# Optimization experiments

Hardware: AMD Instinct MI355X
Metric: run time of the kernel (lower is better)

## Reference

```python
import jax, jax.numpy as jnp
import numpy as np
import math

B, L, H, E = 4, 1024, 8, 64

def setup_inputs() -> dict:
    key = jax.random.key(0)
    kq, kk, kv, ks = jax.random.split(key, 4)
    return {
        "queries": jax.random.normal(kq, (B, L, H, E), dtype=jnp.float32),
        "keys": jax.random.normal(kk, (B, L, H, E), dtype=jnp.float32),
        "values": jax.random.normal(kv, (B, L, H, E), dtype=jnp.float32),
        "sigma": jax.random.normal(ks, (B, L, H), dtype=jnp.float32),
    }

def reference(queries, keys, values, sigma):
    b, l, h, e = queries.shape
    scale = 1.0 / math.sqrt(e)
    # QK^T scores: [B,H,L,S]
    scores = jnp.einsum('blhe,bshe->bhls', queries, keys)
    # triangular causal mask (mask_flag=True, attn_mask=None path)
    causal = jnp.triu(jnp.ones((l, l), dtype=bool), k=1)
    scores = jnp.where(causal[None, None], -jnp.inf, scores)
    attn = scale * scores
    # sigma -> Gaussian prior
    sig = jnp.transpose(sigma, (0, 2, 1))                      # [B,H,L]
    sig = jax.nn.sigmoid(sig * 5.0) + 1e-5
    sig = jnp.power(3.0, sig) - 1.0
    sig = jnp.broadcast_to(sig[..., None], (b, h, l, l))       # [B,H,L,L]
    idx = jnp.arange(l)
    dist = jnp.abs(idx[:, None] - idx[None, :]).astype(jnp.float32)  # [L,L]
    inv_sqrt_2pi = 1.0 / math.sqrt(2.0 * math.pi)
    prior = inv_sqrt_2pi / sig * jnp.exp(-(dist ** 2) / 2.0 / (sig ** 2))
    series = jax.nn.softmax(attn, axis=-1)                     # dropout p=0 -> identity
    V = jnp.einsum('bhls,bshd->blhd', series, values)
    return V, series, prior, sig
```

## Files before the change

### kernel.cpp

```cpp
#include <hip/hip_runtime.h>

typedef __attribute__((ext_vector_type(8))) short bf16x8;
typedef __attribute__((ext_vector_type(4))) float f32x4;

constexpr int NB = 4, NL = 1024, NH = 8, NE = 64, NBH = NB * NH;

constexpr size_t OFF_V      = 0;
constexpr size_t OFF_SERIES = (size_t)NB * NL * NH * NE;
constexpr size_t OFF_PRIOR  = OFF_SERIES + (size_t)NBH * NL * NL;
constexpr size_t OFF_SIG    = OFF_PRIOR  + (size_t)NBH * NL * NL;

__device__ __forceinline__ unsigned short f2bf(float x) {
  unsigned int u = __builtin_bit_cast(unsigned int, x);
  u = (u + 0x7FFFu + ((u >> 16) & 1u)) >> 16;
  return (unsigned short)u;
}

__device__ __forceinline__ f32x4 mfma16(bf16x8 a, bf16x8 b, f32x4 c) {
  return __builtin_amdgcn_mfma_f32_16x16x32_bf16(a, b, c, 0, 0, 0);
}

__global__ __launch_bounds__(256)
void prior_kernel(const float* __restrict__ sigma, float* __restrict__ out) {
  const float inv_sqrt_2pi = 0.39894228040143267f;
  const float ln3 = 1.0986122886681098f;
  float4* __restrict__ prior4  = (float4*)(out + OFF_PRIOR);
  float4* __restrict__ sig4    = (float4*)(out + OFF_SIG);
  float4* __restrict__ series4 = (float4*)(out + OFF_SERIES);

  const int tid  = threadIdx.x;
  const int lane = tid & 63;
  const int rowIdx = blockIdx.x * 4 + (tid >> 6);
  const int l  = rowIdx & 1023;
  const int bh = rowIdx >> 10;
  const int b  = bh >> 3, h = bh & 7;

  const float x    = sigma[((size_t)b * NL + l) * NH + h];
  const float sg   = 1.0f / (1.0f + __expf(-5.0f * x)) + 1e-5f;
  const float sigv = __expf(sg * ln3) - 1.0f;
  const float coef = inv_sqrt_2pi / sigv;
  const float inv2 = -0.5f / (sigv * sigv);

  const size_t rbase = (size_t)rowIdx * (NL / 4);
  const int rbe4 = ((l & ~63) + 64) >> 2;
  const float4 zero4 = make_float4(0.f, 0.f, 0.f, 0.f);
  const float4 sv = make_float4(sigv, sigv, sigv, sigv);

#pragma unroll
  for (int k = 0; k < 4; ++k) {
    const int c  = lane + k * 64;
    const int sb = c * 4;
    const int d0 = l - sb, d1 = l - (sb + 1), d2 = l - (sb + 2), d3 = l - (sb + 3);
    float4 pr;
    pr.x = coef * __expf((float)(d0 * d0) * inv2);
    pr.y = coef * __expf((float)(d1 * d1) * inv2);
    pr.z = coef * __expf((float)(d2 * d2) * inv2);
    pr.w = coef * __expf((float)(d3 * d3) * inv2);
    prior4[rbase + c] = pr;
    sig4[rbase + c]   = sv;
    if (c >= rbe4) series4[rbase + c] = zero4;
  }
}

__device__ __forceinline__ void stage64(const float* __restrict__ src,
                                        unsigned short* lds) {
  const int t = threadIdx.x;
  const int s = t >> 2, q = t & 3;
  const float4* rp = (const float4*)(src + (size_t)s * (NH * NE) + q * 16);
  float4 v0 = rp[0], v1 = rp[1], v2 = rp[2], v3 = rp[3];
  unsigned int u[8];
  u[0] = f2bf(v0.x) | ((unsigned)f2bf(v0.y) << 16);
  u[1] = f2bf(v0.z) | ((unsigned)f2bf(v0.w) << 16);
  u[2] = f2bf(v1.x) | ((unsigned)f2bf(v1.y) << 16);
  u[3] = f2bf(v1.z) | ((unsigned)f2bf(v1.w) << 16);
  u[4] = f2bf(v2.x) | ((unsigned)f2bf(v2.y) << 16);
  u[5] = f2bf(v2.z) | ((unsigned)f2bf(v2.w) << 16);
  u[6] = f2bf(v3.x) | ((unsigned)f2bf(v3.y) << 16);
  u[7] = f2bf(v3.z) | ((unsigned)f2bf(v3.w) << 16);
  const int sw = (s & 7) << 4;
  char* row = (char*)lds + s * 128;
  *(uint4*)(row + ((q * 32)      ^ sw)) = make_uint4(u[0], u[1], u[2], u[3]);
  *(uint4*)(row + ((q * 32 + 16) ^ sw)) = make_uint4(u[4], u[5], u[6], u[7]);
}

__device__ __forceinline__ void stageV(const float* __restrict__ src,
                                       unsigned int* ldsv) {
  const int t = threadIdx.x;
  const int sp = t >> 3;
  const int ec = t & 7;
  const float* r0 = src + (size_t)(2 * sp) * (NH * NE) + ec * 8;
  const float* r1 = r0 + NH * NE;
  float4 a0 = ((const float4*)r0)[0], a1 = ((const float4*)r0)[1];
  float4 b0 = ((const float4*)r1)[0], b1 = ((const float4*)r1)[1];
  unsigned int u[8];
  u[0] = f2bf(a0.x) | ((unsigned)f2bf(b0.x) << 16);
  u[1] = f2bf(a0.y) | ((unsigned)f2bf(b0.y) << 16);
  u[2] = f2bf(a0.z) | ((unsigned)f2bf(b0.z) << 16);
  u[3] = f2bf(a0.w) | ((unsigned)f2bf(b0.w) << 16);
  u[4] = f2bf(a1.x) | ((unsigned)f2bf(b1.x) << 16);
  u[5] = f2bf(a1.y) | ((unsigned)f2bf(b1.y) << 16);
  u[6] = f2bf(a1.z) | ((unsigned)f2bf(b1.z) << 16);
  u[7] = f2bf(a1.w) | ((unsigned)f2bf(b1.w) << 16);
  unsigned int* p = ldsv + sp * 68 + ec * 8;
  *(uint4*)(p)     = make_uint4(u[0], u[1], u[2], u[3]);
  *(uint4*)(p + 4) = make_uint4(u[4], u[5], u[6], u[7]);
}

__device__ __forceinline__ bf16x8 readAB(const unsigned short* lds, int row,
                                         int bytecol) {
  const char* p = (const char*)lds + row * 128 + (bytecol ^ ((row & 7) << 4));
  return *(const bf16x8*)p;
}

__global__ __launch_bounds__(256)
void attn_kernel(const float* __restrict__ Qp, const float* __restrict__ Kp,
                 const float* __restrict__ Vp, float* __restrict__ out) {
  const int blk = blockIdx.x;
  const int bh = blk & 31;
  const int g5 = blk >> 5;
  const int w  = (g5 < 8) ? (15 - g5) : (g5 - 8);
  const int b = bh >> 3, h = bh & 7;

  __shared__ unsigned short ldsQ[64 * 64];
  __shared__ unsigned short ldsK[64 * 64];
  __shared__ unsigned int   ldsV[32 * 68];
  __shared__ unsigned short ldsP[4][16 * 72];
  const int tid  = threadIdx.x;
  const int lane = tid & 63;
  const int wv   = tid >> 6;
  const int g    = lane >> 4;
  const int e0   = lane & 15;

  const size_t rowstride = NH * NE;
  const float* Qbase = Qp + ((size_t)(b * NL + w * 64) * NH + h) * NE;
  const float* Kbase = Kp + ((size_t)(b * NL) * NH + h) * NE;
  const float* Vbase = Vp + ((size_t)(b * NL) * NH + h) * NE;

  stage64(Qbase, ldsQ);
  __syncthreads();

  const bf16x8 aq0 = readAB(ldsQ, wv * 16 + e0, g * 16);
  const bf16x8 aq1 = readAB(ldsQ, wv * 16 + e0, g * 16 + 64);

  const float scale = 0.125f;
  const int r_glob0 = w * 64 + wv * 16 + g * 4;
  float rsum[4] = {0.f, 0.f, 0.f, 0.f};

  for (int st = 0; st <= w; ++st) {
    __syncthreads();
    stage64(Kbase + (size_t)(st * 64) * rowstride, ldsK);
    __syncthreads();
#pragma unroll
    for (int ct = 0; ct < 4; ++ct) {
      f32x4 acc = {0.f, 0.f, 0.f, 0.f};
      bf16x8 bk0 = readAB(ldsK, ct * 16 + e0, g * 16);
      bf16x8 bk1 = readAB(ldsK, ct * 16 + e0, g * 16 + 64);
      acc = mfma16(aq0, bk0, acc);
      acc = mfma16(aq1, bk1, acc);
      const int s_g = st * 64 + ct * 16 + e0;
#pragma unroll
      for (int j = 0; j < 4; ++j) {
        float e = __expf(acc[j] * scale - 20.0f);
        if (s_g > r_glob0 + j) e = 0.f;
        rsum[j] += e;
      }
    }
  }

  float rinv[4];
#pragma unroll
  for (int j = 0; j < 4; ++j) {
    float v = rsum[j];
    v += __shfl_xor(v, 1);
    v += __shfl_xor(v, 2);
    v += __shfl_xor(v, 4);
    v += __shfl_xor(v, 8);
    rinv[j] = 1.0f / v;
  }

  f32x4 acc_o[4];
#pragma unroll
  for (int i = 0; i < 4; ++i) acc_o[i] = f32x4{0.f, 0.f, 0.f, 0.f};

  unsigned short* ldsPw = ldsP[wv];
  float* __restrict__ series = out + OFF_SERIES + (size_t)bh * NL * NL;

  for (int st = 0; st <= w; ++st) {
    __syncthreads();
    stage64(Kbase + (size_t)(st * 64) * rowstride, ldsK);
    stageV (Vbase + (size_t)(st * 64) * rowstride, ldsV);
    __syncthreads();
#pragma unroll
    for (int ct = 0; ct < 4; ++ct) {
      f32x4 acc = {0.f, 0.f, 0.f, 0.f};
      bf16x8 bk0 = readAB(ldsK, ct * 16 + e0, g * 16);
      bf16x8 bk1 = readAB(ldsK, ct * 16 + e0, g * 16 + 64);
      acc = mfma16(aq0, bk0, acc);
      acc = mfma16(aq1, bk1, acc);
      const int s_g = st * 64 + ct * 16 + e0;
#pragma unroll
      for (int j = 0; j < 4; ++j) {
        float e = __expf(acc[j] * scale - 20.0f);
        if (s_g > r_glob0 + j) e = 0.f;
        const float pn = e * rinv[j];
        series[(size_t)(r_glob0 + j) * NL + s_g] = pn;
        ldsPw[(g * 4 + j) * 72 + ct * 16 + e0] = f2bf(pn);
      }
    }
#pragma unroll
    for (int sh = 0; sh < 2; ++sh) {
      const char* pp = (const char*)ldsPw + e0 * 144 + sh * 64 + g * 16;
      const bf16x8 ap = *(const bf16x8*)pp;
#pragma unroll
      for (int ce = 0; ce < 4; ++ce) {
        const unsigned int* vp = ldsV + (sh * 16 + g * 4) * 68 + ce * 16 + e0;
        uint4 vw = make_uint4(vp[0], vp[68], vp[136], vp[204]);
        const bf16x8 bv = __builtin_bit_cast(bf16x8, vw);
        acc_o[ce] = mfma16(ap, bv, acc_o[ce]);
      }
    }
  }

  float* __restrict__ vout = out + OFF_V;
#pragma unroll
  for (int ce = 0; ce < 4; ++ce) {
#pragma unroll
    for (int j = 0; j < 4; ++j) {
      vout[((size_t)(b * NL + r_glob0 + j) * NH + h) * NE + ce * 16 + e0] =
          acc_o[ce][j];
    }
  }
}

extern "C" void kernel_launch(void* const* d_in, const int* in_sizes, int n_in,
                              void* d_out, int out_size, void* d_ws, size_t ws_size,
                              hipStream_t stream) {
  const float* Qp = (const float*)d_in[0];
  const float* Kp = (const float*)d_in[1];
  const float* Vp = (const float*)d_in[2];
  const float* Sg = (const float*)d_in[3];
  float* out = (float*)d_out;
  (void)d_ws; (void)ws_size;

  prior_kernel<<<dim3(NBH * NL / 4), dim3(256), 0, stream>>>(Sg, out);
  attn_kernel <<<dim3(512),          dim3(256), 0, stream>>>(Qp, Kp, Vp, out);
}
```

Baseline: 460.8 us.

## Single-pass attention writing unnormalized series, normalize in prior kernel

Removes the first QK^T pass that only computed row sums. The attention kernel now writes unnormalized exp scores to series and accumulates PV unnormalized, scaling V by the reciprocal sum at the end. It stores per-row reciprocals in the workspace, which the prior kernel (now launched second) uses to rescale series with a read-modify-write. The change also adds register prefetch of the next K/V tile and s_setprio around the PV MFMAs. The cost is an extra read and write of the lower-triangular series in the prior kernel, in exchange for halving the QK^T and exp work.

```diff
diff --git a/kernel.cpp b/kernel.cpp
--- a/kernel.cpp
+++ b/kernel.cpp
@@ -20,8 +20,188 @@
   return __builtin_amdgcn_mfma_f32_16x16x32_bf16(a, b, c, 0, 0, 0);
 }
 
+__device__ __forceinline__ void loadT(const float* __restrict__ src, float4* r) {
+  const int t = threadIdx.x;
+  const int s = t >> 2, q = t & 3;
+  const float4* rp = (const float4*)(src + (size_t)s * (NH * NE) + q * 16);
+  r[0] = rp[0]; r[1] = rp[1]; r[2] = rp[2]; r[3] = rp[3];
+}
+
+__device__ __forceinline__ void writeT(const float4* v, unsigned short* lds) {
+  const int t = threadIdx.x;
+  const int s = t >> 2, q = t & 3;
+  unsigned int u[8];
+  u[0] = f2bf(v[0].x) | ((unsigned)f2bf(v[0].y) << 16);
+  u[1] = f2bf(v[0].z) | ((unsigned)f2bf(v[0].w) << 16);
+  u[2] = f2bf(v[1].x) | ((unsigned)f2bf(v[1].y) << 16);
+  u[3] = f2bf(v[1].z) | ((unsigned)f2bf(v[1].w) << 16);
+  u[4] = f2bf(v[2].x) | ((unsigned)f2bf(v[2].y) << 16);
+  u[5] = f2bf(v[2].z) | ((unsigned)f2bf(v[2].w) << 16);
+  u[6] = f2bf(v[3].x) | ((unsigned)f2bf(v[3].y) << 16);
+  u[7] = f2bf(v[3].z) | ((unsigned)f2bf(v[3].w) << 16);
+  const int sw = (s & 7) << 4;
+  char* row = (char*)lds + s * 128;
+  *(uint4*)(row + ((q * 32)      ^ sw)) = make_uint4(u[0], u[1], u[2], u[3]);
+  *(uint4*)(row + ((q * 32 + 16) ^ sw)) = make_uint4(u[4], u[5], u[6], u[7]);
+}
+
+__device__ __forceinline__ void loadV(const float* __restrict__ src, float4* r) {
+  const int t = threadIdx.x;
+  const int sp = t >> 3, ec = t & 7;
+  const float* r0 = src + (size_t)(2 * sp) * (NH * NE) + ec * 8;
+  const float* r1 = r0 + NH * NE;
+  r[0] = ((const float4*)r0)[0]; r[1] = ((const float4*)r0)[1];
+  r[2] = ((const float4*)r1)[0]; r[3] = ((const float4*)r1)[1];
+}
+
+__device__ __forceinline__ void writeV(const float4* v, unsigned int* ldsv) {
+  const int t = threadIdx.x;
+  const int sp = t >> 3, ec = t & 7;
+  unsigned int u[8];
+  u[0] = f2bf(v[0].x) | ((unsigned)f2bf(v[2].x) << 16);
+  u[1] = f2bf(v[0].y) | ((unsigned)f2bf(v[2].y) << 16);
+  u[2] = f2bf(v[0].z) | ((unsigned)f2bf(v[2].z) << 16);
+  u[3] = f2bf(v[0].w) | ((unsigned)f2bf(v[2].w) << 16);
+  u[4] = f2bf(v[1].x) | ((unsigned)f2bf(v[3].x) << 16);
+  u[5] = f2bf(v[1].y) | ((unsigned)f2bf(v[3].y) << 16);
+  u[6] = f2bf(v[1].z) | ((unsigned)f2bf(v[3].z) << 16);
+  u[7] = f2bf(v[1].w) | ((unsigned)f2bf(v[3].w) << 16);
+  unsigned int* p = ldsv + sp * 68 + ec * 8;
+  *(uint4*)(p)     = make_uint4(u[0], u[1], u[2], u[3]);
+  *(uint4*)(p + 4) = make_uint4(u[4], u[5], u[6], u[7]);
+}
+
+__device__ __forceinline__ void stageQ(const float* __restrict__ src,
+                                       unsigned short* lds) {
+  float4 r[4];
+  loadT(src, r);
+  writeT(r, lds);
+}
+
+__device__ __forceinline__ bf16x8 readAB(const unsigned short* lds, int row,
+                                         int bytecol) {
+  const char* p = (const char*)lds + row * 128 + (bytecol ^ ((row & 7) << 4));
+  return *(const bf16x8*)p;
+}
+
 __global__ __launch_bounds__(256)
-void prior_kernel(const float* __restrict__ sigma, float* __restrict__ out) {
+void attn_kernel(const float* __restrict__ Qp, const float* __restrict__ Kp,
+                 const float* __restrict__ Vp, float* __restrict__ rws,
+                 float* __restrict__ out) {
+  const int blk = blockIdx.x;
+  const int bh = blk & 31;
+  const int g5 = blk >> 5;
+  const int w  = (g5 < 8) ? (15 - g5) : (g5 - 8);
+  const int b = bh >> 3, h = bh & 7;
+
+  __shared__ unsigned short ldsQ[64 * 64];
+  __shared__ unsigned short ldsK[64 * 64];
+  __shared__ unsigned int   ldsV[32 * 68];
+  __shared__ unsigned short ldsP[4][16 * 72];
+
+  const int tid  = threadIdx.x;
+  const int lane = tid & 63;
+  const int wv   = tid >> 6;
+  const int g    = lane >> 4;
+  const int e0   = lane & 15;
+
+  const size_t rowstride = NH * NE;
+  const float* Qbase = Qp + ((size_t)(b * NL + w * 64) * NH + h) * NE;
+  const float* Kbase = Kp + ((size_t)(b * NL) * NH + h) * NE;
+  const float* Vbase = Vp + ((size_t)(b * NL) * NH + h) * NE;
+
+  stageQ(Qbase, ldsQ);
+  __syncthreads();
+
+  const bf16x8 aq0 = readAB(ldsQ, wv * 16 + e0, g * 16);
+  const bf16x8 aq1 = readAB(ldsQ, wv * 16 + e0, g * 16 + 64);
+
+  const float scale = 0.125f;
+  const int r_glob0 = w * 64 + wv * 16 + g * 4;
+  float rsum[4] = {0.f, 0.f, 0.f, 0.f};
+
+  f32x4 acc_o[4];
+#pragma unroll
+  for (int i = 0; i < 4; ++i) acc_o[i] = f32x4{0.f, 0.f, 0.f, 0.f};
+
+  unsigned short* ldsPw = ldsP[wv];
+  float* __restrict__ series = out + OFF_SERIES + (size_t)bh * NL * NL;
+
+  float4 kreg[4], vreg[4];
+  loadT(Kbase, kreg);
+  loadV(Vbase, vreg);
+
+  for (int st = 0; st <= w; ++st) {
+    __syncthreads();
+    writeT(kreg, ldsK);
+    writeV(vreg, ldsV);
+    __syncthreads();
+    if (st < w) {
+      loadT(Kbase + (size_t)((st + 1) * 64) * rowstride, kreg);
+      loadV(Vbase + (size_t)((st + 1) * 64) * rowstride, vreg);
+    }
+#pragma unroll
+    for (int ct = 0; ct < 4; ++ct) {
+      f32x4 acc = {0.f, 0.f, 0.f, 0.f};
+      bf16x8 bk0 = readAB(ldsK, ct * 16 + e0, g * 16);
+      bf16x8 bk1 = readAB(ldsK, ct * 16 + e0, g * 16 + 64);
+      acc = mfma16(aq0, bk0, acc);
+      acc = mfma16(aq1, bk1, acc);
+      const int s_g = st * 64 + ct * 16 + e0;
+#pragma unroll
+      for (int j = 0; j < 4; ++j) {
+        float e = __expf(acc[j] * scale - 20.0f);
+        if (s_g > r_glob0 + j) e = 0.f;
+        rsum[j] += e;
+        series[(size_t)(r_glob0 + j) * NL + s_g] = e;
+        ldsPw[(g * 4 + j) * 72 + ct * 16 + e0] = f2bf(e);
+      }
+    }
+    __builtin_amdgcn_s_setprio(1);
+#pragma unroll
+    for (int sh = 0; sh < 2; ++sh) {
+      const char* pp = (const char*)ldsPw + e0 * 144 + sh * 64 + g * 16;
+      const bf16x8 ap = *(const bf16x8*)pp;
+#pragma unroll
+      for (int ce = 0; ce < 4; ++ce) {
+        const unsigned int* vp = ldsV + (sh * 16 + g * 4) * 68 + ce * 16 + e0;
+        uint4 vw = make_uint4(vp[0], vp[68], vp[136], vp[204]);
+        const bf16x8 bv = __builtin_bit_cast(bf16x8, vw);
+        acc_o[ce] = mfma16(ap, bv, acc_o[ce]);
+      }
+    }
+    __builtin_amdgcn_s_setprio(0);
+  }
+
+  float rinv[4];
+#pragma unroll
+  for (int j = 0; j < 4; ++j) {
+    float v = rsum[j];
+    v += __shfl_xor(v, 1);
+    v += __shfl_xor(v, 2);
+    v += __shfl_xor(v, 4);
+    v += __shfl_xor(v, 8);
+    rinv[j] = 1.0f / v;
+  }
+  if (e0 == 0) {
+#pragma unroll
+    for (int j = 0; j < 4; ++j) rws[(size_t)bh * NL + r_glob0 + j] = rinv[j];
+  }
+
+  float* __restrict__ vout = out + OFF_V;
+#pragma unroll
+  for (int ce = 0; ce < 4; ++ce) {
+#pragma unroll
+    for (int j = 0; j < 4; ++j) {
+      vout[((size_t)(b * NL + r_glob0 + j) * NH + h) * NE + ce * 16 + e0] =
+          acc_o[ce][j] * rinv[j];
+    }
+  }
+}
+
+__global__ __launch_bounds__(256)
+void prior_norm_kernel(const float* __restrict__ sigma,
+                       const float* __restrict__ rws, float* __restrict__ out) {
   const float inv_sqrt_2pi = 0.39894228040143267f;
   const float ln3 = 1.0986122886681098f;
   float4* __restrict__ prior4  = (float4*)(out + OFF_PRIOR);
@@ -40,6 +220,7 @@
   const float sigv = __expf(sg * ln3) - 1.0f;
   const float coef = inv_sqrt_2pi / sigv;
   const float inv2 = -0.5f / (sigv * sigv);
+  const float rinv = rws[rowIdx];
 
   const size_t rbase = (size_t)rowIdx * (NL / 4);
   const int rbe4 = ((l & ~63) + 64) >> 2;
@@ -58,176 +239,12 @@
     pr.w = coef * __expf((float)(d3 * d3) * inv2);
     prior4[rbase + c] = pr;
     sig4[rbase + c]   = sv;
-    if (c >= rbe4) series4[rbase + c] = zero4;
-  }
-}
-
-__device__ __forceinline__ void stage64(const float* __restrict__ src,
-                                        unsigned short* lds) {
-  const int t = threadIdx.x;
-  const int s = t >> 2, q = t & 3;
-  const float4* rp = (const float4*)(src + (size_t)s * (NH * NE) + q * 16);
-  float4 v0 = rp[0], v1 = rp[1], v2 = rp[2], v3 = rp[3];
-  unsigned int u[8];
-  u[0] = f2bf(v0.x) | ((unsigned)f2bf(v0.y) << 16);
-  u[1] = f2bf(v0.z) | ((unsigned)f2bf(v0.w) << 16);
-  u[2] = f2bf(v1.x) | ((unsigned)f2bf(v1.y) << 16);
-  u[3] = f2bf(v1.z) | ((unsigned)f2bf(v1.w) << 16);
-  u[4] = f2bf(v2.x) | ((unsigned)f2bf(v2.y) << 16);
-  u[5] = f2bf(v2.z) | ((unsigned)f2bf(v2.w) << 16);
-  u[6] = f2bf(v3.x) | ((unsigned)f2bf(v3.y) << 16);
-  u[7] = f2bf(v3.z) | ((unsigned)f2bf(v3.w) << 16);
-  const int sw = (s & 7) << 4;
-  char* row = (char*)lds + s * 128;
-  *(uint4*)(row + ((q * 32)      ^ sw)) = make_uint4(u[0], u[1], u[2], u[3]);
-  *(uint4*)(row + ((q * 32 + 16) ^ sw)) = make_uint4(u[4], u[5], u[6], u[7]);
-}
-
-__device__ __forceinline__ void stageV(const float* __restrict__ src,
-                                       unsigned int* ldsv) {
-  const int t = threadIdx.x;
-  const int sp = t >> 3;
-  const int ec = t & 7;
-  const float* r0 = src + (size_t)(2 * sp) * (NH * NE) + ec * 8;
-  const float* r1 = r0 + NH * NE;
-  float4 a0 = ((const float4*)r0)[0], a1 = ((const float4*)r0)[1];
-  float4 b0 = ((const float4*)r1)[0], b1 = ((const float4*)r1)[1];
-  unsigned int u[8];
-  u[0] = f2bf(a0.x) | ((unsigned)f2bf(b0.x) << 16);
-  u[1] = f2bf(a0.y) | ((unsigned)f2bf(b0.y) << 16);
-  u[2] = f2bf(a0.z) | ((unsigned)f2bf(b0.z) << 16);
-  u[3] = f2bf(a0.w) | ((unsigned)f2bf(b0.w) << 16);
-  u[4] = f2bf(a1.x) | ((unsigned)f2bf(b1.x) << 16);
-  u[5] = f2bf(a1.y) | ((unsigned)f2bf(b1.y) << 16);
-  u[6] = f2bf(a1.z) | ((unsigned)f2bf(b1.z) << 16);
-  u[7] = f2bf(a1.w) | ((unsigned)f2bf(b1.w) << 16);
-  unsigned int* p = ldsv + sp * 68 + ec * 8;
-  *(uint4*)(p)     = make_uint4(u[0], u[1], u[2], u[3]);
-  *(uint4*)(p + 4) = make_uint4(u[4], u[5], u[6], u[7]);
-}
-
-__device__ __forceinline__ bf16x8 readAB(const unsigned short* lds, int row,
-                                         int bytecol) {
-  const char* p = (const char*)lds + row * 128 + (bytecol ^ ((row & 7) << 4));
-  return *(const bf16x8*)p;
-}
-
-__global__ __launch_bounds__(256)
-void attn_kernel(const float* __restrict__ Qp, const float* __restrict__ Kp,
-                 const float* __restrict__ Vp, float* __restrict__ out) {
-  const int blk = blockIdx.x;
-  const int bh = blk & 31;
-  const int g5 = blk >> 5;
-  const int w  = (g5 < 8) ? (15 - g5) : (g5 - 8);
-  const int b = bh >> 3, h = bh & 7;
-
-  __shared__ unsigned short ldsQ[64 * 64];
-  __shared__ unsigned short ldsK[64 * 64];
-  __shared__ unsigned int   ldsV[32 * 68];
-  __shared__ unsigned short ldsP[4][16 * 72];
-  const int tid  = threadIdx.x;
-  const int lane = tid & 63;
-  const int wv   = tid >> 6;
-  const int g    = lane >> 4;
-  const int e0   = lane & 15;
-
-  const size_t rowstride = NH * NE;
-  const float* Qbase = Qp + ((size_t)(b * NL + w * 64) * NH + h) * NE;
-  const float* Kbase = Kp + ((size_t)(b * NL) * NH + h) * NE;
-  const float* Vbase = Vp + ((size_t)(b * NL) * NH + h) * NE;
-
-  stage64(Qbase, ldsQ);
-  __syncthreads();
-
-  const bf16x8 aq0 = readAB(ldsQ, wv * 16 + e0, g * 16);
-  const bf16x8 aq1 = readAB(ldsQ, wv * 16 + e0, g * 16 + 64);
-
-  const float scale = 0.125f;
-  const int r_glob0 = w * 64 + wv * 16 + g * 4;
-  float rsum[4] = {0.f, 0.f, 0.f, 0.f};
-
-  for (int st = 0; st <= w; ++st) {
-    __syncthreads();
-    stage64(Kbase + (size_t)(st * 64) * rowstride, ldsK);
-    __syncthreads();
-#pragma unroll
-    for (int ct = 0; ct < 4; ++ct) {
-      f32x4 acc = {0.f, 0.f, 0.f, 0.f};
-      bf16x8 bk0 = readAB(ldsK, ct * 16 + e0, g * 16);
-      bf16x8 bk1 = readAB(ldsK, ct * 16 + e0, g * 16 + 64);
-      acc = mfma16(aq0, bk0, acc);
-      acc = mfma16(aq1, bk1, acc);
-      const int s_g = st * 64 + ct * 16 + e0;
-#pragma unroll
-      for (int j = 0; j < 4; ++j) {
-        float e = __expf(acc[j] * scale - 20.0f);
-        if (s_g > r_glob0 + j) e = 0.f;
-        rsum[j] += e;
-      }
-    }
-  }
-
-  float rinv[4];
-#pragma unroll
-  for (int j = 0; j < 4; ++j) {
-    float v = rsum[j];
-    v += __shfl_xor(v, 1);
-    v += __shfl_xor(v, 2);
-    v += __shfl_xor(v, 4);
-    v += __shfl_xor(v, 8);
-    rinv[j] = 1.0f / v;
-  }
-
-  f32x4 acc_o[4];
-#pragma unroll
-  for (int i = 0; i < 4; ++i) acc_o[i] = f32x4{0.f, 0.f, 0.f, 0.f};
-
-  unsigned short* ldsPw = ldsP[wv];
-  float* __restrict__ series = out + OFF_SERIES + (size_t)bh * NL * NL;
-
-  for (int st = 0; st <= w; ++st) {
-    __syncthreads();
-    stage64(Kbase + (size_t)(st * 64) * rowstride, ldsK);
-    stageV (Vbase + (size_t)(st * 64) * rowstride, ldsV);
-    __syncthreads();
-#pragma unroll
-    for (int ct = 0; ct < 4; ++ct) {
-      f32x4 acc = {0.f, 0.f, 0.f, 0.f};
-      bf16x8 bk0 = readAB(ldsK, ct * 16 + e0, g * 16);
-      bf16x8 bk1 = readAB(ldsK, ct * 16 + e0, g * 16 + 64);
-      acc = mfma16(aq0, bk0, acc);
-      acc = mfma16(aq1, bk1, acc);
-      const int s_g = st * 64 + ct * 16 + e0;
-#pragma unroll
-      for (int j = 0; j < 4; ++j) {
-        float e = __expf(acc[j] * scale - 20.0f);
-        if (s_g > r_glob0 + j) e = 0.f;
-        const float pn = e * rinv[j];
-        series[(size_t)(r_glob0 + j) * NL + s_g] = pn;
-        ldsPw[(g * 4 + j) * 72 + ct * 16 + e0] = f2bf(pn);
-      }
-    }
-#pragma unroll
-    for (int sh = 0; sh < 2; ++sh) {
-      const char* pp = (const char*)ldsPw + e0 * 144 + sh * 64 + g * 16;
-      const bf16x8 ap = *(const bf16x8*)pp;
-#pragma unroll
-      for (int ce = 0; ce < 4; ++ce) {
-        const unsigned int* vp = ldsV + (sh * 16 + g * 4) * 68 + ce * 16 + e0;
-        uint4 vw = make_uint4(vp[0], vp[68], vp[136], vp[204]);
-        const bf16x8 bv = __builtin_bit_cast(bf16x8, vw);
-        acc_o[ce] = mfma16(ap, bv, acc_o[ce]);
-      }
-    }
-  }
-
-  float* __restrict__ vout = out + OFF_V;
-#pragma unroll
-  for (int ce = 0; ce < 4; ++ce) {
-#pragma unroll
-    for (int j = 0; j < 4; ++j) {
-      vout[((size_t)(b * NL + r_glob0 + j) * NH + h) * NE + ce * 16 + e0] =
-          acc_o[ce][j];
+    if (c >= rbe4) {
+      series4[rbase + c] = zero4;
+    } else {
+      float4 v = series4[rbase + c];
+      v.x *= rinv; v.y *= rinv; v.z *= rinv; v.w *= rinv;
+      series4[rbase + c] = v;
     }
   }
 }
@@ -240,8 +257,8 @@
   const float* Vp = (const float*)d_in[2];
   const float* Sg = (const float*)d_in[3];
   float* out = (float*)d_out;
-  (void)d_ws; (void)ws_size;
-
-  prior_kernel<<<dim3(NBH * NL / 4), dim3(256), 0, stream>>>(Sg, out);
-  attn_kernel <<<dim3(512),          dim3(256), 0, stream>>>(Qp, Kp, Vp, out);
-}
+  float* rws = (float*)d_ws;
+
+  attn_kernel      <<<dim3(512),          dim3(256), 0, stream>>>(Qp, Kp, Vp, rws, out);
+  prior_norm_kernel<<<dim3(NBH * NL / 4), dim3(256), 0, stream>>>(Sg, rws, out);
+}
```

Measured after the change: 460.1 us. About the same (-0.1%).
